# Kernel tuning notes

Measured on AMD Instinct MI355X. Metric: run time of the kernel, lower is better.

The kernel has to match this reference:

```python
import jax, jax.numpy as jnp
import numpy as np

TOP_K = 2


def setup_inputs() -> dict:
    key = jax.random.key(0)
    k1, k2, k3, k4 = jax.random.split(key, 4)
    B, L, D, F, E = 4, 2048, 1024, 4096, 8
    x = jax.random.normal(k1, (B, L, D), dtype=jnp.float32)
    router_w = jax.random.normal(k2, (D, E), dtype=jnp.float32) * (1.0 / np.sqrt(D))
    w1 = jax.random.normal(k3, (E, D, F), dtype=jnp.float32) * (1.0 / np.sqrt(D))
    w2 = jax.random.normal(k4, (E, F, D), dtype=jnp.float32) * (1.0 / np.sqrt(F))
    return {"x": x, "router_w": router_w, "w1": w1, "w2": w2}


def reference(x, router_w, w1, w2):
    # x: [B, L, D]; router_w: [D, E]; w1: [E, D, F]; w2: [E, F, D]
    B, L, D = x.shape
    E = router_w.shape[1]
    xt = x.reshape(-1, D)                       # [T, D], T = B*L
    router_logits = xt @ router_w               # [T, E] router GEMM
    probs = jax.nn.softmax(router_logits, axis=-1)
    top_w, top_i = jax.lax.top_k(probs, TOP_K)  # [T, k]
    top_w = top_w / jnp.sum(top_w, axis=-1, keepdims=True)  # renormalize top-k
    # dense combine gates: [T, E], zero outside the selected experts
    gates = jnp.sum(jax.nn.one_hot(top_i, E, dtype=xt.dtype) * top_w[..., None], axis=1)
    out = jnp.zeros_like(xt)
    for e in range(E):  # fixed small expert loop (structurally distinct params)
        h = jax.nn.gelu(xt @ w1[e])             # [T, F]
        out = out + gates[:, e:e + 1] * (h @ w2[e])
    return out.reshape(B, L, D)
```

## Files before the change

kernel.cpp:

```cpp
#include <hip/hip_runtime.h>
#include <hip/hip_bf16.h>


#define T_TOK 8192
#define DDIM  1024
#define FDIM  4096
#define NEXP  8
#define RTOT  (T_TOK * 2)
#define RPAD  (RTOT + 128)

#define BM 128
#define BN 128
#define BK 64

typedef __bf16 bf16x8 __attribute__((ext_vector_type(8)));
typedef float  f32x4  __attribute__((ext_vector_type(4)));

__device__ __forceinline__ float gelu_tanh(float x) {
  float u = 0.7978845608028654f * (x + 0.044715f * x * x * x);
  return __fdividef(x, 1.f + __expf(-2.f * u));
}

#define GLOBAL_TO_LDS16(gp, lp)                                                   \
  __builtin_amdgcn_global_load_lds((const __attribute__((address_space(1))) void*)(gp), \
                                   (__attribute__((address_space(3))) void*)(lp), 16, 0, 0)

__global__ __launch_bounds__(256) void transpose_cast_both(const float* __restrict__ w1,
                                                           const float* __restrict__ w2,
                                                           __hip_bfloat16* __restrict__ w1t,
                                                           __hip_bfloat16* __restrict__ w2t) {
  __shared__ __hip_bfloat16 tile[64 * 66];
  int bid = blockIdx.x;
  const float* in; __hip_bfloat16* outp; int Rr, Cc;
  if (bid < NEXP * 1024) { in = w1; outp = w1t; Rr = DDIM; Cc = FDIM; }
  else { bid -= NEXP * 1024; in = w2; outp = w2t; Rr = FDIM; Cc = DDIM; }
  int tilesC = Cc >> 6;
  int per = (Rr >> 6) * tilesC;
  int e = bid / per, rem = bid % per;
  int tr = rem / tilesC, tc = rem % tilesC;
  const float* ip = in + (size_t)e * Rr * Cc + (size_t)(tr * 64) * Cc + tc * 64;
  __hip_bfloat16* op = outp + (size_t)e * Rr * Cc + (size_t)(tc * 64) * Rr + tr * 64;
  int tid = threadIdx.x;
  int lrow = tid >> 4, lcol = (tid & 15) * 4;
#pragma unroll
  for (int p = 0; p < 4; p++) {
    int r = p * 16 + lrow;
    float4 v = *(const float4*)(ip + (size_t)r * Cc + lcol);
    tile[r * 66 + lcol + 0] = __float2bfloat16(v.x);
    tile[r * 66 + lcol + 1] = __float2bfloat16(v.y);
    tile[r * 66 + lcol + 2] = __float2bfloat16(v.z);
    tile[r * 66 + lcol + 3] = __float2bfloat16(v.w);
  }
  __syncthreads();
  int orow_l = tid >> 3, ocol = (tid & 7) * 8;
#pragma unroll
  for (int p = 0; p < 2; p++) {
    int orow = p * 32 + orow_l;
    union { __hip_bfloat16 h[8]; uint4 u; } pk;
#pragma unroll
    for (int j = 0; j < 8; j++) pk.h[j] = tile[(ocol + j) * 66 + orow];
    *(uint4*)(op + (size_t)orow * Rr + ocol) = pk.u;
  }
}

__global__ __launch_bounds__(256) void router_kernel(const float* __restrict__ x,
                                                     const float* __restrict__ rw,
                                                     int* __restrict__ counts,
                                                     int* __restrict__ pair_e,
                                                     int* __restrict__ pair_slot,
                                                     float* __restrict__ pair_gate) {
  int lane = threadIdx.x & 63;
  int wid = threadIdx.x >> 6;
  int t = blockIdx.x * 4 + wid;
  const float* xr = x + (size_t)t * DDIM;
  float acc[NEXP];
#pragma unroll
  for (int e = 0; e < NEXP; e++) acc[e] = 0.f;
  for (int d0 = lane * 4; d0 < DDIM; d0 += 256) {
    float4 xv = *(const float4*)(xr + d0);
    const float* r0 = rw + (size_t)d0 * NEXP;
#pragma unroll
    for (int e = 0; e < NEXP; e++)
      acc[e] += xv.x * r0[e] + xv.y * r0[NEXP + e] + xv.z * r0[2 * NEXP + e] + xv.w * r0[3 * NEXP + e];
  }
#pragma unroll
  for (int e = 0; e < NEXP; e++) {
#pragma unroll
    for (int m = 32; m > 0; m >>= 1) acc[e] += __shfl_xor(acc[e], m, 64);
  }
  if (lane == 0) {
    int e1 = 0; float l1 = acc[0];
    for (int e = 1; e < NEXP; e++) if (acc[e] > l1) { l1 = acc[e]; e1 = e; }
    int e2 = -1; float l2 = -1e30f;
    for (int e = 0; e < NEXP; e++) { if (e == e1) continue; if (acc[e] > l2) { l2 = acc[e]; e2 = e; } }
    float g1 = 1.f / (1.f + __expf(l2 - l1));
    float g2 = 1.f - g1;
    int s1 = atomicAdd(&counts[e1], 1);
    int s2 = atomicAdd(&counts[e2], 1);
    pair_e[2 * t] = e1;     pair_slot[2 * t] = s1;     pair_gate[2 * t] = g1;
    pair_e[2 * t + 1] = e2; pair_slot[2 * t + 1] = s2; pair_gate[2 * t + 1] = g2;
  }
}

__global__ __launch_bounds__(256) void gather_kernel(const float* __restrict__ x,
                                                     const int* __restrict__ counts,
                                                     const int* __restrict__ pair_e,
                                                     const int* __restrict__ pair_slot,
                                                     const float* __restrict__ pair_gate,
                                                     __hip_bfloat16* __restrict__ Xg,
                                                     int* __restrict__ trow,
                                                     float* __restrict__ row_gate) {
  int p = blockIdx.x;
  int t = p >> 1;
  int e = pair_e[p];
  int base = 0;
#pragma unroll
  for (int i = 0; i < NEXP; i++) base += (i < e) ? counts[i] : 0;
  int row = base + pair_slot[p];
  const float* xr = x + (size_t)t * DDIM;
  __hip_bfloat16* dst = Xg + (size_t)row * DDIM;
  int i = threadIdx.x * 4;
  float4 v = *(const float4*)(xr + i);
  union { ushort4 u; __hip_bfloat16 h[4]; } o;
  o.h[0] = __float2bfloat16(v.x);
  o.h[1] = __float2bfloat16(v.y);
  o.h[2] = __float2bfloat16(v.z);
  o.h[3] = __float2bfloat16(v.w);
  *(ushort4*)(dst + i) = o.u;
  if (threadIdx.x == 0) { trow[p] = row; row_gate[row] = pair_gate[p]; }
}

template <int EPI>
__global__ __launch_bounds__(256) void moe_gemm(const __hip_bfloat16* __restrict__ A,
                                                const __hip_bfloat16* __restrict__ Bw,
                                                __hip_bfloat16* __restrict__ Hout,
                                                float* __restrict__ Cout,
                                                const int* __restrict__ counts,
                                                const float* __restrict__ row_gate,
                                                int K, int N) {
  const int MT = T_TOK / BM;
  const int NT = N / BN;
  int bid = blockIdx.x;
  int e = bid / (MT * NT);
  int rem = bid % (MT * NT);
  const int GM = 8;
  int width = GM * NT;
  int group = rem / width;
  int gm0 = group * GM;
  int gsize = (MT - gm0 < GM) ? (MT - gm0) : GM;
  int mt = gm0 + (rem % gsize);
  int nt = (rem % width) / gsize;

  int n_e = counts[e];
  if (mt * BM >= n_e) return;
  int row0 = 0;
  for (int i = 0; i < NEXP; i++) row0 += (i < e) ? counts[i] : 0;
  int m_start = row0 + mt * BM;
  int row_end = row0 + n_e;

  const __hip_bfloat16* Abase = A + (size_t)m_start * K;
  const __hip_bfloat16* Bbase = Bw + (size_t)e * N * K + (size_t)(nt * BN) * K;

  __shared__ alignas(16) __hip_bfloat16 As[BM * BK];
  __shared__ alignas(16) __hip_bfloat16 Bs[BN * BK];

  int tid = threadIdx.x;
  int lane = tid & 63, wid = tid >> 6;
  int wm = (wid >> 1) * 64, wn = (wid & 1) * 64;
  int lr = lane & 15;
  int kq8 = (lane >> 4);

  f32x4 acc[4][4];
#pragma unroll
  for (int i = 0; i < 4; i++)
#pragma unroll
    for (int j = 0; j < 4; j++)
#pragma unroll
      for (int r = 0; r < 4; r++) acc[i][j][r] = 0.f;

  for (int kt = 0; kt < K; kt += BK) {
#pragma unroll
    for (int i = 0; i < 4; i++) {
      int q = i * 256 + tid;
      int r = q >> 3, c = (q & 7) ^ (r & 7);
      GLOBAL_TO_LDS16(Abase + (size_t)r * K + kt + c * 8, As + (size_t)(i * 256 + wid * 64) * 8);
    }
#pragma unroll
    for (int i = 0; i < 4; i++) {
      int q = i * 256 + tid;
      int r = q >> 3, c = (q & 7) ^ (r & 7);
      GLOBAL_TO_LDS16(Bbase + (size_t)r * K + kt + c * 8, Bs + (size_t)(i * 256 + wid * 64) * 8);
    }
    __syncthreads();
#pragma unroll
    for (int kk = 0; kk < BK; kk += 32) {
      int kc = (kk >> 3) + kq8;
      bf16x8 af[4], bfr[4];
#pragma unroll
      for (int i = 0; i < 4; i++) {
        int R = wm + i * 16 + lr;
        af[i] = *(const bf16x8*)(As + R * BK + ((kc ^ (R & 7)) * 8));
      }
#pragma unroll
      for (int j = 0; j < 4; j++) {
        int R = wn + j * 16 + lr;
        bfr[j] = *(const bf16x8*)(Bs + R * BK + ((kc ^ (R & 7)) * 8));
      }
#pragma unroll
      for (int i = 0; i < 4; i++)
#pragma unroll
        for (int j = 0; j < 4; j++)
          acc[i][j] = __builtin_amdgcn_mfma_f32_16x16x32_bf16(af[i], bfr[j], acc[i][j], 0, 0, 0);
    }
    __syncthreads();
  }

  int quad = (lane >> 4) * 4;
#pragma unroll
  for (int i = 0; i < 4; i++) {
#pragma unroll
    for (int r = 0; r < 4; r++) {
      int grow = m_start + wm + i * 16 + quad + r;
      if (grow < row_end) {
        size_t basei = (size_t)grow * N + nt * BN + wn + lr;
        if (EPI == 0) {
#pragma unroll
          for (int j = 0; j < 4; j++)
            Hout[basei + j * 16] = __float2bfloat16(gelu_tanh(acc[i][j][r]));
        } else {
          float g = row_gate[grow];
#pragma unroll
          for (int j = 0; j < 4; j++)
            Cout[basei + j * 16] = g * acc[i][j][r];
        }
      }
    }
  }
}

__global__ __launch_bounds__(256) void combine_kernel(const float* __restrict__ P,
                                                      const int* __restrict__ trow,
                                                      float* __restrict__ out) {
  int t = blockIdx.x;
  int r1 = trow[2 * t], r2 = trow[2 * t + 1];
  int d = threadIdx.x * 4;
  float4 a = *(const float4*)(P + (size_t)r1 * DDIM + d);
  float4 b = *(const float4*)(P + (size_t)r2 * DDIM + d);
  float4 o;
  o.x = a.x + b.x; o.y = a.y + b.y; o.z = a.z + b.z; o.w = a.w + b.w;
  *(float4*)(out + (size_t)t * DDIM + d) = o;
}

extern "C" void kernel_launch(void* const* d_in, const int* in_sizes, int n_in,
                              void* d_out, int out_size, void* d_ws, size_t ws_size,
                              hipStream_t stream) {
  (void)in_sizes; (void)n_in; (void)out_size; (void)ws_size;
  const float* x  = (const float*)d_in[0];
  const float* rw = (const float*)d_in[1];
  const float* w1 = (const float*)d_in[2];
  const float* w2 = (const float*)d_in[3];
  float* out = (float*)d_out;

  char* ws = (char*)d_ws;
  size_t off = 0;
  auto alloc = [&](size_t bytes) -> char* {
    off = (off + 255) & ~(size_t)255;
    char* p = ws + off;
    off += bytes;
    return p;
  };
  int*   counts    = (int*)alloc(NEXP * 4);
  int*   pair_e    = (int*)alloc((size_t)RTOT * 4);
  int*   pair_slot = (int*)alloc((size_t)RTOT * 4);
  float* pair_gate = (float*)alloc((size_t)RTOT * 4);
  int*   trow      = (int*)alloc((size_t)RTOT * 4);
  float* row_gate  = (float*)alloc((size_t)RTOT * 4);
  __hip_bfloat16* Xg  = (__hip_bfloat16*)alloc((size_t)RPAD * DDIM * 2);
  __hip_bfloat16* w1t = (__hip_bfloat16*)alloc((size_t)NEXP * DDIM * FDIM * 2);
  __hip_bfloat16* w2t = (__hip_bfloat16*)alloc((size_t)NEXP * DDIM * FDIM * 2);
  __hip_bfloat16* H   = (__hip_bfloat16*)alloc((size_t)RPAD * FDIM * 2);
  float* P = (float*)w1t;

  hipMemsetAsync(counts, 0, NEXP * 4, stream);

  transpose_cast_both<<<2 * NEXP * 1024, 256, 0, stream>>>(w1, w2, w1t, w2t);
  router_kernel<<<T_TOK / 4, 256, 0, stream>>>(x, rw, counts, pair_e, pair_slot, pair_gate);
  gather_kernel<<<RTOT, 256, 0, stream>>>(x, counts, pair_e, pair_slot, pair_gate, Xg, trow, row_gate);

  moe_gemm<0><<<NEXP * (T_TOK / BM) * (FDIM / BN), 256, 0, stream>>>(
      Xg, w1t, H, nullptr, counts, nullptr, DDIM, FDIM);
  moe_gemm<1><<<NEXP * (T_TOK / BM) * (DDIM / BN), 256, 0, stream>>>(
      H, w2t, nullptr, P, counts, row_gate, FDIM, DDIM);
  combine_kernel<<<T_TOK, 256, 0, stream>>>(P, trow, out);
}
```

Before: 944.4 us.

## Rework weight transpose, hoist GEMM addressing, and store expert partials as bf16

```diff
diff --git a/kernel.cpp b/kernel.cpp
--- a/kernel.cpp
+++ b/kernel.cpp
@@ -17,8 +17,13 @@
 typedef float  f32x4  __attribute__((ext_vector_type(4)));
 
 __device__ __forceinline__ float gelu_tanh(float x) {
-  float u = 0.7978845608028654f * (x + 0.044715f * x * x * x);
+  float x2 = x * x;
+  float u = x * (0.7978845608028654f + 0.0356774081f * x2);
   return __fdividef(x, 1.f + __expf(-2.f * u));
+}
+
+__device__ __forceinline__ float b2f(unsigned short u) {
+  return __uint_as_float(((unsigned)u) << 16);
 }
 
 #define GLOBAL_TO_LDS16(gp, lp)                                                   \
@@ -29,7 +34,7 @@
                                                            const float* __restrict__ w2,
                                                            __hip_bfloat16* __restrict__ w1t,
                                                            __hip_bfloat16* __restrict__ w2t) {
-  __shared__ __hip_bfloat16 tile[64 * 66];
+  __shared__ __hip_bfloat16 tileT[64 * 72];
   int bid = blockIdx.x;
   const float* in; __hip_bfloat16* outp; int Rr, Cc;
   if (bid < NEXP * 1024) { in = w1; outp = w1t; Rr = DDIM; Cc = FDIM; }
@@ -41,26 +46,31 @@
   const float* ip = in + (size_t)e * Rr * Cc + (size_t)(tr * 64) * Cc + tc * 64;
   __hip_bfloat16* op = outp + (size_t)e * Rr * Cc + (size_t)(tc * 64) * Rr + tr * 64;
   int tid = threadIdx.x;
-  int lrow = tid >> 4, lcol = (tid & 15) * 4;
-#pragma unroll
-  for (int p = 0; p < 4; p++) {
-    int r = p * 16 + lrow;
-    float4 v = *(const float4*)(ip + (size_t)r * Cc + lcol);
-    tile[r * 66 + lcol + 0] = __float2bfloat16(v.x);
-    tile[r * 66 + lcol + 1] = __float2bfloat16(v.y);
-    tile[r * 66 + lcol + 2] = __float2bfloat16(v.z);
-    tile[r * 66 + lcol + 3] = __float2bfloat16(v.w);
+  int cbase = (tid & 15) * 4;
+  int rbase = (tid >> 4) * 2;
+#pragma unroll
+  for (int p = 0; p < 2; p++) {
+    int r0 = rbase + p * 32;
+    float4 va = *(const float4*)(ip + (size_t)r0 * Cc + cbase);
+    float4 vb = *(const float4*)(ip + (size_t)(r0 + 1) * Cc + cbase);
+    const float* fa = &va.x;
+    const float* fb = &vb.x;
+#pragma unroll
+    for (int i = 0; i < 4; i++) {
+      union { __hip_bfloat16 h[2]; unsigned u; } pk;
+      pk.h[0] = __float2bfloat16(fa[i]);
+      pk.h[1] = __float2bfloat16(fb[i]);
+      *(unsigned*)(&tileT[(cbase + i) * 72 + r0]) = pk.u;
+    }
   }
   __syncthreads();
-  int orow_l = tid >> 3, ocol = (tid & 7) * 8;
-#pragma unroll
-  for (int p = 0; p < 2; p++) {
-    int orow = p * 32 + orow_l;
-    union { __hip_bfloat16 h[8]; uint4 u; } pk;
-#pragma unroll
-    for (int j = 0; j < 8; j++) pk.h[j] = tile[(ocol + j) * 66 + orow];
-    *(uint4*)(op + (size_t)orow * Rr + ocol) = pk.u;
-  }
+  int rr = tid >> 2, sb = (tid & 3) * 16;
+  const __hip_bfloat16* src = tileT + rr * 72 + sb;
+  __hip_bfloat16* dst = op + (size_t)rr * Rr + sb;
+  uint4 v0 = *(const uint4*)(src);
+  uint4 v1 = *(const uint4*)(src + 8);
+  *(uint4*)(dst) = v0;
+  *(uint4*)(dst + 8) = v1;
 }
 
 __global__ __launch_bounds__(256) void router_kernel(const float* __restrict__ x,
@@ -133,8 +143,7 @@
 template <int EPI>
 __global__ __launch_bounds__(256) void moe_gemm(const __hip_bfloat16* __restrict__ A,
                                                 const __hip_bfloat16* __restrict__ Bw,
-                                                __hip_bfloat16* __restrict__ Hout,
-                                                float* __restrict__ Cout,
+                                                __hip_bfloat16* __restrict__ Pout,
                                                 const int* __restrict__ counts,
                                                 const float* __restrict__ row_gate,
                                                 int K, int N) {
@@ -170,6 +179,28 @@
   int lr = lane & 15;
   int kq8 = (lane >> 4);
 
+  int offA[4][2], offB[4][2];
+#pragma unroll
+  for (int i = 0; i < 4; i++) {
+    int Ra = wm + i * 16 + lr;
+    int Rb = wn + i * 16 + lr;
+#pragma unroll
+    for (int h = 0; h < 2; h++) {
+      int kc = kq8 + h * 4;
+      offA[i][h] = Ra * BK + ((kc ^ (Ra & 7)) * 8);
+      offB[i][h] = Rb * BK + ((kc ^ (Rb & 7)) * 8);
+    }
+  }
+  const __hip_bfloat16* ga[4];
+  const __hip_bfloat16* gb[4];
+#pragma unroll
+  for (int i = 0; i < 4; i++) {
+    int q = i * 256 + tid;
+    int r = q >> 3, c = (q & 7) ^ (r & 7);
+    ga[i] = Abase + (size_t)r * K + c * 8;
+    gb[i] = Bbase + (size_t)r * K + c * 8;
+  }
+
   f32x4 acc[4][4];
 #pragma unroll
   for (int i = 0; i < 4; i++)
@@ -180,32 +211,19 @@
 
   for (int kt = 0; kt < K; kt += BK) {
 #pragma unroll
-    for (int i = 0; i < 4; i++) {
-      int q = i * 256 + tid;
-      int r = q >> 3, c = (q & 7) ^ (r & 7);
-      GLOBAL_TO_LDS16(Abase + (size_t)r * K + kt + c * 8, As + (size_t)(i * 256 + wid * 64) * 8);
-    }
-#pragma unroll
-    for (int i = 0; i < 4; i++) {
-      int q = i * 256 + tid;
-      int r = q >> 3, c = (q & 7) ^ (r & 7);
-      GLOBAL_TO_LDS16(Bbase + (size_t)r * K + kt + c * 8, Bs + (size_t)(i * 256 + wid * 64) * 8);
-    }
+    for (int i = 0; i < 4; i++) GLOBAL_TO_LDS16(ga[i], As + (size_t)(i * 256 + wid * 64) * 8);
+#pragma unroll
+    for (int i = 0; i < 4; i++) GLOBAL_TO_LDS16(gb[i], Bs + (size_t)(i * 256 + wid * 64) * 8);
+#pragma unroll
+    for (int i = 0; i < 4; i++) { ga[i] += BK; gb[i] += BK; }
     __syncthreads();
 #pragma unroll
-    for (int kk = 0; kk < BK; kk += 32) {
-      int kc = (kk >> 3) + kq8;
+    for (int h = 0; h < 2; h++) {
       bf16x8 af[4], bfr[4];
 #pragma unroll
-      for (int i = 0; i < 4; i++) {
-        int R = wm + i * 16 + lr;
-        af[i] = *(const bf16x8*)(As + R * BK + ((kc ^ (R & 7)) * 8));
-      }
-#pragma unroll
-      for (int j = 0; j < 4; j++) {
-        int R = wn + j * 16 + lr;
-        bfr[j] = *(const bf16x8*)(Bs + R * BK + ((kc ^ (R & 7)) * 8));
-      }
+      for (int i = 0; i < 4; i++) af[i] = *(const bf16x8*)(As + offA[i][h]);
+#pragma unroll
+      for (int j = 0; j < 4; j++) bfr[j] = *(const bf16x8*)(Bs + offB[j][h]);
 #pragma unroll
       for (int i = 0; i < 4; i++)
 #pragma unroll
@@ -222,32 +240,35 @@
     for (int r = 0; r < 4; r++) {
       int grow = m_start + wm + i * 16 + quad + r;
       if (grow < row_end) {
-        size_t basei = (size_t)grow * N + nt * BN + wn + lr;
+        __hip_bfloat16* pp = Pout + (size_t)grow * N + nt * BN + wn + lr;
         if (EPI == 0) {
 #pragma unroll
           for (int j = 0; j < 4; j++)
-            Hout[basei + j * 16] = __float2bfloat16(gelu_tanh(acc[i][j][r]));
+            pp[j * 16] = __float2bfloat16(gelu_tanh(acc[i][j][r]));
         } else {
           float g = row_gate[grow];
 #pragma unroll
           for (int j = 0; j < 4; j++)
-            Cout[basei + j * 16] = g * acc[i][j][r];
+            pp[j * 16] = __float2bfloat16(g * acc[i][j][r]);
         }
       }
     }
   }
 }
 
-__global__ __launch_bounds__(256) void combine_kernel(const float* __restrict__ P,
+__global__ __launch_bounds__(256) void combine_kernel(const __hip_bfloat16* __restrict__ P,
                                                       const int* __restrict__ trow,
                                                       float* __restrict__ out) {
   int t = blockIdx.x;
   int r1 = trow[2 * t], r2 = trow[2 * t + 1];
   int d = threadIdx.x * 4;
-  float4 a = *(const float4*)(P + (size_t)r1 * DDIM + d);
-  float4 b = *(const float4*)(P + (size_t)r2 * DDIM + d);
+  ushort4 a = *(const ushort4*)(P + (size_t)r1 * DDIM + d);
+  ushort4 b = *(const ushort4*)(P + (size_t)r2 * DDIM + d);
   float4 o;
-  o.x = a.x + b.x; o.y = a.y + b.y; o.z = a.z + b.z; o.w = a.w + b.w;
+  o.x = b2f(a.x) + b2f(b.x);
+  o.y = b2f(a.y) + b2f(b.y);
+  o.z = b2f(a.z) + b2f(b.z);
+  o.w = b2f(a.w) + b2f(b.w);
   *(float4*)(out + (size_t)t * DDIM + d) = o;
 }
 
@@ -279,7 +300,7 @@
   __hip_bfloat16* w1t = (__hip_bfloat16*)alloc((size_t)NEXP * DDIM * FDIM * 2);
   __hip_bfloat16* w2t = (__hip_bfloat16*)alloc((size_t)NEXP * DDIM * FDIM * 2);
   __hip_bfloat16* H   = (__hip_bfloat16*)alloc((size_t)RPAD * FDIM * 2);
-  float* P = (float*)w1t;
+  __hip_bfloat16* P = w1t;
 
   hipMemsetAsync(counts, 0, NEXP * 4, stream);
 
@@ -288,8 +309,8 @@
   gather_kernel<<<RTOT, 256, 0, stream>>>(x, counts, pair_e, pair_slot, pair_gate, Xg, trow, row_gate);
 
   moe_gemm<0><<<NEXP * (T_TOK / BM) * (FDIM / BN), 256, 0, stream>>>(
-      Xg, w1t, H, nullptr, counts, nullptr, DDIM, FDIM);
+      Xg, w1t, H, counts, nullptr, DDIM, FDIM);
   moe_gemm<1><<<NEXP * (T_TOK / BM) * (DDIM / BN), 256, 0, stream>>>(
-      H, w2t, nullptr, P, counts, row_gate, FDIM, DDIM);
+      H, w2t, P, counts, row_gate, FDIM, DDIM);
   combine_kernel<<<T_TOK, 256, 0, stream>>>(P, trow, out);
 }
```

New measurement: 948.8 us. Within noise of the previous version (+0.5%).
